# Kernel tuning notes

Measured on AMD Instinct MI355X. Metric: run time of the kernel, lower is better.

## Reference

```python
import jax, jax.numpy as jnp
import numpy as np

L, D, H, T_MAX, V = 6, 1024, 16, 1024, 50257
HD = D // H
EPS = 1e-5


def setup_inputs() -> dict:
    key = jax.random.key(0)
    ks = jax.random.split(key, 12)
    s = 0.02
    return {
        "idx": jax.random.randint(ks[0], (2, 1024), 0, V, dtype=jnp.int32),
        "tok_W": jax.random.normal(ks[1], (V, D), jnp.float32) * s,
        "pos_W": jax.random.normal(ks[2], (T_MAX, D), jnp.float32) * s,
        "ln1_g": jnp.ones((L, D), jnp.float32),
        "ln1_b": jnp.zeros((L, D), jnp.float32),
        "Wq": jax.random.normal(ks[3], (L, D, D), jnp.float32) * s,
        "Wk": jax.random.normal(ks[4], (L, D, D), jnp.float32) * s,
        "Wv": jax.random.normal(ks[5], (L, D, D), jnp.float32) * s,
        "Wo": jax.random.normal(ks[6], (L, D, D), jnp.float32) * s,
        "bo": jnp.zeros((L, D), jnp.float32),
        "ln2_g": jnp.ones((L, D), jnp.float32),
        "ln2_b": jnp.zeros((L, D), jnp.float32),
        "W1": jax.random.normal(ks[7], (L, D, 4 * D), jnp.float32) * s,
        "b1": jnp.zeros((L, 4 * D), jnp.float32),
        "W2": jax.random.normal(ks[8], (L, 4 * D, D), jnp.float32) * s,
        "b2": jnp.zeros((L, D), jnp.float32),
        "lnf_g": jnp.ones((D,), jnp.float32),
        "lnf_b": jnp.zeros((D,), jnp.float32),
    }


def _ln(x, g, b):
    mu = jnp.mean(x, axis=-1, keepdims=True)
    var = jnp.mean(jnp.square(x - mu), axis=-1, keepdims=True)
    return (x - mu) * jax.lax.rsqrt(var + EPS) * g + b


def reference(idx, tok_W, pos_W, ln1_g, ln1_b, Wq, Wk, Wv, Wo, bo,
              ln2_g, ln2_b, W1, b1, W2, b2, lnf_g, lnf_b):
    B, T = idx.shape
    x = tok_W[idx] + pos_W[:T]  # [B,T,D]
    mask = jnp.tril(jnp.ones((T, T), bool))

    def block(x, p):
        (g1, b1n, wq, wk, wv, wo, bob, g2, b2n, w1, bb1, w2, bb2) = p
        h = _ln(x, g1, b1n)
        q = (h @ wq).reshape(B, T, H, HD)
        k = (h @ wk).reshape(B, T, H, HD)
        v = (h @ wv).reshape(B, T, H, HD)
        scores = jnp.einsum('bqhd,bkhd->bhqk', q, k) * (HD ** -0.5)
        scores = jnp.where(mask, scores, -jnp.inf)
        wei = jax.nn.softmax(scores, axis=-1)
        att = jnp.einsum('bhqk,bkhd->bqhd', wei, v).reshape(B, T, D)
        x = x + att @ wo + bob
        h2 = _ln(x, g2, b2n)
        ff = jax.nn.gelu(h2 @ w1 + bb1, approximate=False) @ w2 + bb2
        return x + ff, None

    params = (ln1_g, ln1_b, Wq, Wk, Wv, Wo, bo, ln2_g, ln2_b, W1, b1, W2, b2)
    x, _ = jax.lax.scan(block, x, params)
    x = _ln(x, lnf_g, lnf_b)
    logits = x @ tok_W.T  # weight-tied lm_head
    return logits
```

## Files before the change

kernel.cpp:

```cpp
#include <hip/hip_runtime.h>
#include <hip/hip_bf16.h>
#include <math.h>


using u16 = unsigned short;
typedef __attribute__((ext_vector_type(4))) float f32x4;
typedef __attribute__((ext_vector_type(8))) short s16x8;

static __device__ __forceinline__ u16 f2b(float f) {
    __hip_bfloat16 h = __float2bfloat16(f);
    return *reinterpret_cast<u16*>(&h);
}
static __device__ __forceinline__ float b2f(u16 u) {
    __hip_bfloat16 h = *reinterpret_cast<__hip_bfloat16*>(&u);
    return __bfloat162float(h);
}

__global__ __launch_bounds__(256) void gemm_bt(
    const u16* __restrict__ A, const u16* __restrict__ Bt,
    float* __restrict__ Cf, u16* __restrict__ Cb,
    const float* __restrict__ bias, const float* __restrict__ resid,
    int M, int N, int K, int lda, int ldb, int ldc,
    long long aO, long long aI, long long bO, long long bI,
    long long cO, long long cI, int ZH, float scale, int flags)
{
    __shared__ u16 As[128 * 32];
    __shared__ u16 Bs[128 * 32];

    const int t = threadIdx.x;
    const int lane = t & 63, wave = t >> 6;
    const int wm = wave >> 1, wn = wave & 1;
    const int lr = lane & 15, lq = lane >> 4;
    const int n0 = blockIdx.x * 128;
    const int m0 = blockIdx.y * 128;
    const int zb = blockIdx.z / ZH, zh = blockIdx.z % ZH;
    const long long offA = (long long)zb * aO + (long long)zh * aI;
    const long long offB = (long long)zb * bO + (long long)zh * bI;
    const long long offC = (long long)zb * cO + (long long)zh * cI;

    f32x4 acc[4][4];
#pragma unroll
    for (int i = 0; i < 4; i++)
#pragma unroll
        for (int j = 0; j < 4; j++) acc[i][j] = (f32x4){0.f, 0.f, 0.f, 0.f};

    const int e0 = t * 8;
    const int r0 = e0 >> 5;
    const int kk0 = e0 & 31;

    for (int k0 = 0; k0 < K; k0 += 32) {
        __syncthreads();
        {
            const u16* ap = A + offA + (size_t)(m0 + r0) * lda + (k0 + kk0);
            *(uint4*)&As[r0 * 32 + kk0] = *(const uint4*)ap;
            const u16* ap2 = ap + (size_t)64 * lda;
            *(uint4*)&As[(r0 + 64) * 32 + kk0] = *(const uint4*)ap2;
        }
        {
            uint4 z4 = {0, 0, 0, 0};
            int nr = n0 + r0;
            const u16* bp = Bt + offB + (size_t)nr * ldb + (k0 + kk0);
            uint4 v0 = (nr < N) ? *(const uint4*)bp : z4;
            *(uint4*)&Bs[r0 * 32 + kk0] = v0;
            int nr2 = nr + 64;
            const u16* bp2 = bp + (size_t)64 * ldb;
            uint4 v1 = (nr2 < N) ? *(const uint4*)bp2 : z4;
            *(uint4*)&Bs[(r0 + 64) * 32 + kk0] = v1;
        }
        __syncthreads();

        s16x8 a[4], b[4];
#pragma unroll
        for (int i = 0; i < 4; i++)
            a[i] = *(const s16x8*)&As[(wm * 64 + i * 16 + lr) * 32 + lq * 8];
#pragma unroll
        for (int j = 0; j < 4; j++)
            b[j] = *(const s16x8*)&Bs[(wn * 64 + j * 16 + lr) * 32 + lq * 8];
#pragma unroll
        for (int i = 0; i < 4; i++)
#pragma unroll
            for (int j = 0; j < 4; j++)
                acc[i][j] = __builtin_amdgcn_mfma_f32_16x16x32_bf16(
                    a[i], b[j], acc[i][j], 0, 0, 0);
    }

    const bool obf = (flags & 1) != 0;
    const bool gel = (flags & 2) != 0;
#pragma unroll
    for (int i = 0; i < 4; i++) {
#pragma unroll
        for (int j = 0; j < 4; j++) {
            int col = n0 + wn * 64 + j * 16 + lr;
            if (col >= N) continue;
#pragma unroll
            for (int r = 0; r < 4; r++) {
                int row = m0 + wm * 64 + i * 16 + lq * 4 + r;
                float v = acc[i][j][r] * scale;
                if (bias) v += bias[col];
                if (gel) v = 0.5f * v * (1.f + erff(v * 0.70710678118f));
                long long ci = offC + (long long)row * ldc + col;
                if (resid) v += resid[ci];
                if (obf) Cb[ci] = f2b(v);
                else     Cf[ci] = v;
            }
        }
    }
}

__global__ __launch_bounds__(256) void transpose_conv(
    const void* __restrict__ in, u16* __restrict__ out,
    int R, int C, int ldi, int ldo, long long zi, long long zo, int in_bf16)
{
    __shared__ float tile[32][33];
    int tx = threadIdx.x & 31, ty = threadIdx.x >> 5;
    int r0 = blockIdx.y * 32, c0 = blockIdx.x * 32;
    long long ioff = (long long)blockIdx.z * zi;
    long long ooff = (long long)blockIdx.z * zo;
#pragma unroll
    for (int i = 0; i < 32; i += 8) {
        long long r = r0 + ty + i, c = c0 + tx;
        float v;
        if (in_bf16) v = b2f(((const u16*)in)[ioff + r * ldi + c]);
        else         v = ((const float*)in)[ioff + r * ldi + c];
        tile[ty + i][tx] = v;
    }
    __syncthreads();
#pragma unroll
    for (int i = 0; i < 32; i += 8) {
        long long c = c0 + ty + i, r = r0 + tx;
        out[ooff + c * ldo + r] = f2b(tile[tx][ty + i]);
    }
}

__global__ __launch_bounds__(256) void conv_f2b(
    const float* __restrict__ in, u16* __restrict__ out, size_t n)
{
    size_t i = ((size_t)blockIdx.x * 256 + threadIdx.x) * 4;
    if (i >= n) return;
    float4 f = *(const float4*)&in[i];
    out[i + 0] = f2b(f.x);
    out[i + 1] = f2b(f.y);
    out[i + 2] = f2b(f.z);
    out[i + 3] = f2b(f.w);
}

__global__ __launch_bounds__(256) void embed_k(
    const int* __restrict__ idx, const float* __restrict__ tokW,
    const float* __restrict__ posW, float* __restrict__ x)
{
    int row = blockIdx.x;
    int tt = row & 1023;
    int tok = idx[row];
    int c = threadIdx.x * 4;
    float4 a = *(const float4*)&tokW[(size_t)tok * 1024 + c];
    float4 p = *(const float4*)&posW[(size_t)tt * 1024 + c];
    float4 r = {a.x + p.x, a.y + p.y, a.z + p.z, a.w + p.w};
    *(float4*)&x[(size_t)row * 1024 + c] = r;
}

__global__ __launch_bounds__(256) void ln_k(
    const float* __restrict__ x, const float* __restrict__ g,
    const float* __restrict__ b, u16* __restrict__ out)
{
    __shared__ float sbuf[8];
    int row = blockIdx.x;
    int c = threadIdx.x * 4;
    float4 v = *(const float4*)&x[(size_t)row * 1024 + c];
    float s = v.x + v.y + v.z + v.w;
    float s2 = v.x * v.x + v.y * v.y + v.z * v.z + v.w * v.w;
#pragma unroll
    for (int o = 32; o > 0; o >>= 1) {
        s += __shfl_down(s, o, 64);
        s2 += __shfl_down(s2, o, 64);
    }
    int lane = threadIdx.x & 63, wave = threadIdx.x >> 6;
    if (lane == 0) { sbuf[wave] = s; sbuf[4 + wave] = s2; }
    __syncthreads();
    float mean = (sbuf[0] + sbuf[1] + sbuf[2] + sbuf[3]) * (1.f / 1024.f);
    float m2 = (sbuf[4] + sbuf[5] + sbuf[6] + sbuf[7]) * (1.f / 1024.f);
    float rstd = rsqrtf(m2 - mean * mean + 1e-5f);
    float vals[4] = {v.x, v.y, v.z, v.w};
    u16 o4[4];
#pragma unroll
    for (int i = 0; i < 4; i++) {
        float y = (vals[i] - mean) * rstd * g[c + i] + b[c + i];
        o4[i] = f2b(y);
    }
    *(uint2*)&out[(size_t)row * 1024 + c] = *(uint2*)o4;
}

__global__ __launch_bounds__(256) void softmax_causal(u16* __restrict__ S)
{
    __shared__ float sbuf[8];
    int row = blockIdx.x;
    int q = row & 1023;
    u16* p = S + (size_t)row * 1024;
    int c = threadIdx.x * 4;
    u16 u4[4];
    *(uint2*)u4 = *(const uint2*)&p[c];
    float v[4];
#pragma unroll
    for (int i = 0; i < 4; i++) v[i] = (c + i <= q) ? b2f(u4[i]) : -1e30f;
    float mx = fmaxf(fmaxf(v[0], v[1]), fmaxf(v[2], v[3]));
#pragma unroll
    for (int o = 32; o > 0; o >>= 1) mx = fmaxf(mx, __shfl_down(mx, o, 64));
    int lane = threadIdx.x & 63, wave = threadIdx.x >> 6;
    if (lane == 0) sbuf[wave] = mx;
    __syncthreads();
    mx = fmaxf(fmaxf(sbuf[0], sbuf[1]), fmaxf(sbuf[2], sbuf[3]));
    float e[4], sum = 0.f;
#pragma unroll
    for (int i = 0; i < 4; i++) {
        e[i] = (c + i <= q) ? expf(v[i] - mx) : 0.f;
        sum += e[i];
    }
#pragma unroll
    for (int o = 32; o > 0; o >>= 1) sum += __shfl_down(sum, o, 64);
    if (lane == 0) sbuf[4 + wave] = sum;
    __syncthreads();
    float inv = 1.f / (sbuf[4] + sbuf[5] + sbuf[6] + sbuf[7]);
#pragma unroll
    for (int i = 0; i < 4; i++) u4[i] = f2b(e[i] * inv);
    *(uint2*)&p[c] = *(uint2*)u4;
}

extern "C" void kernel_launch(void* const* d_in, const int* in_sizes, int n_in,
                              void* d_out, int out_size, void* d_ws, size_t ws_size,
                              hipStream_t stream)
{
    const int*   idx  = (const int*)d_in[0];
    const float* tokW = (const float*)d_in[1];
    const float* posW = (const float*)d_in[2];
    const float* ln1g = (const float*)d_in[3];
    const float* ln1b = (const float*)d_in[4];
    const float* Wq   = (const float*)d_in[5];
    const float* Wk   = (const float*)d_in[6];
    const float* Wv   = (const float*)d_in[7];
    const float* Wo   = (const float*)d_in[8];
    const float* bo   = (const float*)d_in[9];
    const float* ln2g = (const float*)d_in[10];
    const float* ln2b = (const float*)d_in[11];
    const float* W1   = (const float*)d_in[12];
    const float* b1   = (const float*)d_in[13];
    const float* W2   = (const float*)d_in[14];
    const float* b2   = (const float*)d_in[15];
    const float* lnfg = (const float*)d_in[16];
    const float* lnfb = (const float*)d_in[17];
    float* out = (float*)d_out;

    char* w = (char*)d_ws;
    auto alloc = [&](size_t bytes) -> char* {
        char* p = w;
        w += (bytes + 255) & ~(size_t)255;
        return p;
    };
    float* x    = (float*)alloc(2048ull * 1024 * 4);
    u16* h      = (u16*)alloc(2048ull * 1024 * 2);
    u16* qkv    = (u16*)alloc(2048ull * 3072 * 2);
    u16* vt     = (u16*)alloc(2ull * 1024 * 1024 * 2);
    u16* attb   = (u16*)alloc(2048ull * 1024 * 2);
    u16* ffb    = (u16*)alloc(2048ull * 4096 * 2);
    u16* wqkvT  = (u16*)alloc(3072ull * 1024 * 2);
    u16* woT    = (u16*)alloc(1024ull * 1024 * 2);
    u16* w1T    = (u16*)alloc(4096ull * 1024 * 2);
    u16* w2T    = (u16*)alloc(1024ull * 4096 * 2);
    u16* S      = (u16*)alloc(50257ull * 1024 * 2);
    u16* twb    = S;

    auto gemm = [&](const u16* A, const u16* Bt, float* Cf, u16* Cb,
                    const float* bias, const float* resid,
                    int M, int N, int K, int lda, int ldb, int ldc,
                    long long aO, long long aI, long long bO, long long bI,
                    long long cO, long long cI, int Z, int ZH,
                    float scale, int flags) {
        dim3 g((N + 127) / 128, M / 128, Z);
        gemm_bt<<<g, dim3(256), 0, stream>>>(A, Bt, Cf, Cb, bias, resid,
                                             M, N, K, lda, ldb, ldc,
                                             aO, aI, bO, bI, cO, cI,
                                             ZH, scale, flags);
    };

    embed_k<<<2048, 256, 0, stream>>>(idx, tokW, posW, x);

    const long long TT = 1024ll * 1024;
    for (int l = 0; l < 6; l++) {
        const float* wq = Wq + (size_t)l * 1024 * 1024;
        const float* wk = Wk + (size_t)l * 1024 * 1024;
        const float* wv = Wv + (size_t)l * 1024 * 1024;
        const float* wo = Wo + (size_t)l * 1024 * 1024;
        const float* w1 = W1 + (size_t)l * 1024 * 4096;
        const float* w2 = W2 + (size_t)l * 4096 * 1024;

        dim3 tg(32, 32, 1);
        transpose_conv<<<tg, 256, 0, stream>>>(wq, wqkvT,            1024, 1024, 1024, 1024, 0, 0, 0);
        transpose_conv<<<tg, 256, 0, stream>>>(wk, wqkvT + 1048576,  1024, 1024, 1024, 1024, 0, 0, 0);
        transpose_conv<<<tg, 256, 0, stream>>>(wv, wqkvT + 2097152,  1024, 1024, 1024, 1024, 0, 0, 0);
        transpose_conv<<<tg, 256, 0, stream>>>(wo, woT,              1024, 1024, 1024, 1024, 0, 0, 0);
        transpose_conv<<<dim3(128, 32, 1), 256, 0, stream>>>(w1, w1T, 1024, 4096, 4096, 1024, 0, 0, 0);
        transpose_conv<<<dim3(32, 128, 1), 256, 0, stream>>>(w2, w2T, 4096, 1024, 1024, 4096, 0, 0, 0);

        ln_k<<<2048, 256, 0, stream>>>(x, ln1g + l * 1024, ln1b + l * 1024, h);
        gemm(h, wqkvT, nullptr, qkv, nullptr, nullptr,
             2048, 3072, 1024, 1024, 1024, 3072,
             0, 0, 0, 0, 0, 0, 1, 1, 1.f, 1);
        transpose_conv<<<dim3(32, 32, 2), 256, 0, stream>>>(
            qkv + 2048, vt, 1024, 1024, 3072, 1024,
            1024ll * 3072, TT, 1);
        gemm(qkv, qkv + 1024, nullptr, S, nullptr, nullptr,
             1024, 1024, 64, 3072, 3072, 1024,
             1024ll * 3072, 64, 1024ll * 3072, 64, 16 * TT, TT,
             32, 16, 0.125f, 1);
        softmax_causal<<<32768, 256, 0, stream>>>(S);
        gemm(S, vt, nullptr, attb, nullptr, nullptr,
             1024, 64, 1024, 1024, 1024, 1024,
             16 * TT, TT, TT, 64ll * 1024, TT, 64,
             32, 16, 1.f, 1);
        gemm(attb, woT, x, nullptr, bo + l * 1024, x,
             2048, 1024, 1024, 1024, 1024, 1024,
             0, 0, 0, 0, 0, 0, 1, 1, 1.f, 0);
        ln_k<<<2048, 256, 0, stream>>>(x, ln2g + l * 1024, ln2b + l * 1024, h);
        gemm(h, w1T, nullptr, ffb, b1 + l * 4096, nullptr,
             2048, 4096, 1024, 1024, 1024, 4096,
             0, 0, 0, 0, 0, 0, 1, 1, 1.f, 1 | 2);
        gemm(ffb, w2T, x, nullptr, b2 + l * 1024, x,
             2048, 1024, 4096, 4096, 4096, 1024,
             0, 0, 0, 0, 0, 0, 1, 1, 1.f, 0);
    }

    ln_k<<<2048, 256, 0, stream>>>(x, lnfg, lnfb, h);
    conv_f2b<<<50257, 256, 0, stream>>>(tokW, twb, 50257ull * 1024);
    gemm(h, twb, out, nullptr, nullptr, nullptr,
         2048, 50257, 1024, 1024, 1024, 50257,
         0, 0, 0, 0, 0, 0, 1, 1, 1.f, 0);
}
```

Measured before the change: 3.754 ms.

## Load GEMM tiles directly into LDS and swap grid block order

Replaces the register-staged global-to-shared copies in the GEMM with direct global_load_lds transfers, so data no longer passes through VGPRs on its way to LDS. Out-of-range B rows are clamped to the last valid row rather than zero-filled, which stays correct only if those extra columns are never stored. The grid is also transposed so consecutive blocks walk along M and share the same B (weight) tile, which is meant to improve L2 reuse of the large lm_head weight. The LDS layout relies on per-wave contiguous 1KB chunks matching the previous row-major tile layout.

New measurement: 3.293 ms. -12.3%, faster.

```diff
diff --git a/kernel.cpp b/kernel.cpp
--- a/kernel.cpp
+++ b/kernel.cpp
@@ -15,6 +15,10 @@
     __hip_bfloat16 h = *reinterpret_cast<__hip_bfloat16*>(&u);
     return __bfloat162float(h);
 }
+
+#define GLDS16(gp, lp) __builtin_amdgcn_global_load_lds( \
+    (const __attribute__((address_space(1))) unsigned int*)(gp), \
+    (__attribute__((address_space(3))) unsigned int*)(lp), 16, 0, 0)
 
 __global__ __launch_bounds__(256) void gemm_bt(
     const u16* __restrict__ A, const u16* __restrict__ Bt,
@@ -31,8 +35,8 @@
     const int lane = t & 63, wave = t >> 6;
     const int wm = wave >> 1, wn = wave & 1;
     const int lr = lane & 15, lq = lane >> 4;
-    const int n0 = blockIdx.x * 128;
-    const int m0 = blockIdx.y * 128;
+    const int m0 = blockIdx.x * 128;
+    const int n0 = blockIdx.y * 128;
     const int zb = blockIdx.z / ZH, zh = blockIdx.z % ZH;
     const long long offA = (long long)zb * aO + (long long)zh * aI;
     const long long offB = (long long)zb * bO + (long long)zh * bI;
@@ -44,28 +48,24 @@
 #pragma unroll
         for (int j = 0; j < 4; j++) acc[i][j] = (f32x4){0.f, 0.f, 0.f, 0.f};
 
-    const int e0 = t * 8;
-    const int r0 = e0 >> 5;
-    const int kk0 = e0 & 31;
+    const int r0 = t >> 2;
+    const int kk0 = (t & 3) << 3;
+    const int wvb = wave << 10;
 
     for (int k0 = 0; k0 < K; k0 += 32) {
         __syncthreads();
         {
             const u16* ap = A + offA + (size_t)(m0 + r0) * lda + (k0 + kk0);
-            *(uint4*)&As[r0 * 32 + kk0] = *(const uint4*)ap;
-            const u16* ap2 = ap + (size_t)64 * lda;
-            *(uint4*)&As[(r0 + 64) * 32 + kk0] = *(const uint4*)ap2;
+            GLDS16(ap, (char*)As + wvb);
+            GLDS16(ap + (size_t)64 * lda, (char*)As + 4096 + wvb);
         }
         {
-            uint4 z4 = {0, 0, 0, 0};
-            int nr = n0 + r0;
-            const u16* bp = Bt + offB + (size_t)nr * ldb + (k0 + kk0);
-            uint4 v0 = (nr < N) ? *(const uint4*)bp : z4;
-            *(uint4*)&Bs[r0 * 32 + kk0] = v0;
-            int nr2 = nr + 64;
-            const u16* bp2 = bp + (size_t)64 * ldb;
-            uint4 v1 = (nr2 < N) ? *(const uint4*)bp2 : z4;
-            *(uint4*)&Bs[(r0 + 64) * 32 + kk0] = v1;
+            int nr  = n0 + r0;      if (nr  >= N) nr  = N - 1;
+            int nr2 = n0 + r0 + 64; if (nr2 >= N) nr2 = N - 1;
+            const u16* bp  = Bt + offB + (size_t)nr  * ldb + (k0 + kk0);
+            const u16* bp2 = Bt + offB + (size_t)nr2 * ldb + (k0 + kk0);
+            GLDS16(bp,  (char*)Bs + wvb);
+            GLDS16(bp2, (char*)Bs + 4096 + wvb);
         }
         __syncthreads();
 
@@ -273,7 +273,7 @@
                     long long aO, long long aI, long long bO, long long bI,
                     long long cO, long long cI, int Z, int ZH,
                     float scale, int flags) {
-        dim3 g((N + 127) / 128, M / 128, Z);
+        dim3 g(M / 128, (N + 127) / 128, Z);
         gemm_bt<<<g, dim3(256), 0, stream>>>(A, Bt, Cf, Cb, bias, resid,
                                              M, N, K, lda, ldb, ldc,
                                              aO, aI, bO, bI, cO, cI,
```
